# Kernel tuning notes

Measured on AMD Instinct MI355X. Metric: run time of the kernel, lower is better.

Reference implementation:

```python
import jax, jax.numpy as jnp
import numpy as np

RADIUS = 0.2
NSAMPLE = 32


def setup_inputs() -> dict:
    key = jax.random.key(0)
    k1, k2 = jax.random.split(key)
    B, N = 8, 4096
    xyz = jax.random.uniform(k1, (B, N, 3), dtype=jnp.float32)
    xyz_new = jax.random.uniform(k2, (B, N, 3), dtype=jnp.float32)  # ignored by forward, kept for signature fidelity
    return {"xyz": xyz, "xyz_new": xyz_new}


def _ball_query(radius, nsample, xyz, new_xyz):
    # xyz: [B, N, 3] source points; new_xyz: [B, M, 3] query centers.
    # Returns idx: [B, M, nsample] int32, matching pointnet2 CUDA ball_query:
    # first `nsample` indices j (in increasing j order) with ||q - p_j||^2 < r^2;
    # unused slots are filled with the first valid index.
    B, N, _ = xyz.shape
    sq_src = jnp.sum(xyz * xyz, axis=-1)          # [B, N]
    sq_q = jnp.sum(new_xyz * new_xyz, axis=-1)    # [B, M]
    # d2[b, m, n] = ||q_m - p_n||^2
    d2 = sq_q[:, :, None] + sq_src[:, None, :] - 2.0 * jnp.einsum(
        "bmc,bnc->bmn", new_xyz, xyz)             # [B, M, N]
    mask = d2 < (radius * radius)                 # [B, M, N] bool
    # key = index j when within radius, else sentinel N (sorts to the end)
    idx_range = jnp.arange(N, dtype=jnp.int32)
    keys = jnp.where(mask, idx_range[None, None, :], jnp.int32(N))
    sorted_keys = jnp.sort(keys, axis=-1)[..., :nsample]  # [B, M, nsample]
    first = sorted_keys[..., 0:1]                 # first valid index (pad value)
    idx = jnp.where(sorted_keys < N, sorted_keys, first)
    return idx.astype(jnp.int32)


def reference(xyz, xyz_new):
    # Faithful to the module: ball_query(radius, nsample, xyz, xyz) — xyz_new unused.
    return _ball_query(RADIUS, NSAMPLE, xyz, xyz)
```

## Files before the change

kernel.cpp:

```cpp
#include <hip/hip_runtime.h>
#include <cstdint>


#define BQ_N   4096
#define BQ_B   8
#define BQ_NS  32
#define BQ_R2  0.04f

__device__ __forceinline__ float sq_plain(float x, float y, float z) {
    float r, t;
    asm("v_mul_f32 %0, %2, %2\n\t"
        "v_mul_f32 %1, %3, %3\n\t"
        "v_add_f32 %0, %0, %1\n\t"
        "v_mul_f32 %1, %4, %4\n\t"
        "v_add_f32 %0, %0, %1"
        : "=&v"(r), "=&v"(t)
        : "v"(x), "v"(y), "v"(z));
    return r;
}

__device__ __forceinline__ float d2_mixed_s(float qx, float qy, float qz,
                                            float sqq,
                                            float sx, float sy, float sz,
                                            float sqs) {
    float r, t;
    asm("v_mul_f32 %0, %2, %5\n\t"
        "v_fma_f32 %0, %3, %6, %0\n\t"
        "v_fma_f32 %0, %4, %7, %0\n\t"
        "v_add_f32 %0, %0, %0\n\t"
        "v_add_f32 %1, %8, %9\n\t"
        "v_sub_f32 %0, %1, %0"
        : "=&v"(r), "=&v"(t)
        : "s"(qx), "s"(qy), "s"(qz), "v"(sx), "v"(sy), "v"(sz),
          "s"(sqq), "v"(sqs));
    return r;
}

__device__ __forceinline__ float rfl(float v) {
    return __int_as_float(__builtin_amdgcn_readfirstlane(__float_as_int(v)));
}

__device__ __forceinline__ float gfun(float q) {
    float t = fminf(q, 1.0f - q) * 5.0f;
    t = fminf(t, 1.0f);
    return 0.5f + (0.75f - 0.25f * t * t) * t;
}

__device__ __forceinline__ void emit_query(int* orow, int lane, uint64_t word) {
    const int cnt = __popcll(word);
    int incl = cnt;
    #pragma unroll
    for (int off = 1; off < 64; off <<= 1) {
        const int t = __shfl_up(incl, off);
        if (lane >= off) incl += t;
    }
    const int pre   = incl - cnt;
    const int total = __shfl(incl, 63);

    int first;
    const uint64_t nz = __ballot(word != 0ull);
    if (nz == 0ull) {
        first = BQ_N;
    } else {
        const int fl = __builtin_ctzll(nz);
        const uint64_t fw = __shfl(word, fl);
        first = (fl << 6) + __builtin_ctzll(fw);
    }

    uint64_t w = word;
    int pos = pre;
    while (w != 0ull && pos < BQ_NS) {
        const int bit = __builtin_ctzll(w);
        orow[pos] = (lane << 6) + bit;
        w &= (w - 1);
        ++pos;
    }
    if (lane >= total && lane < BQ_NS) orow[lane] = first;
}

__global__ __launch_bounds__(512, 4)
void ball_query_kernel(const float* __restrict__ xyz, int* __restrict__ out)
{
    __shared__ float4 pts[BQ_N];

    const int b     = blockIdx.x >> 6;
    const int qbase = (blockIdx.x & 63) << 6;
    const float* __restrict__ src = xyz + (size_t)b * BQ_N * 3;
    const int lane = threadIdx.x & 63;
    const int wid  = threadIdx.x >> 6;
    int* __restrict__ outb = out + (size_t)(b * BQ_N) * BQ_NS;

    unsigned long long v;
    {
        const int m = qbase + lane;
        const float x = src[3 * m + 0];
        const float y = src[3 * m + 1];
        const float z = src[3 * m + 2];
        const float key = gfun(x) * gfun(y) * gfun(z);
        v = ((unsigned long long)__float_as_uint(key) << 32) | (unsigned)lane;
    }
    #pragma unroll
    for (int k = 2; k <= 64; k <<= 1) {
        #pragma unroll
        for (int j = k >> 1; j > 0; j >>= 1) {
            const unsigned long long o = __shfl_xor(v, j);
            const bool up       = ((lane & k) == 0);
            const bool take_min = (((lane & j) == 0) == up);
            const bool less     = (v < o);
            v = (less == take_min) ? v : o;
        }
    }
    int qlocal[8];
    #pragma unroll
    for (int j = 0; j < 8; ++j)
        qlocal[j] = (int)(__shfl(v, (wid << 3) + j) & 0xffffffffull) & 63;

    for (int j = threadIdx.x; j < BQ_N; j += 512) {
        const float x = src[3 * j + 0];
        const float y = src[3 * j + 1];
        const float z = src[3 * j + 2];
        pts[j] = make_float4(x, y, z, sq_plain(x, y, z));
    }
    __syncthreads();

    float qx[8], qy[8], qz[8], qw[8];
    #pragma unroll
    for (int j = 0; j < 8; ++j) {
        const float4 Qj = pts[qbase + qlocal[j]];
        qx[j] = rfl(Qj.x); qy[j] = rfl(Qj.y);
        qz[j] = rfl(Qj.z); qw[j] = rfl(Qj.w);
    }

    uint64_t W[8] = {0, 0, 0, 0, 0, 0, 0, 0};
    int      F[8] = {0, 0, 0, 0, 0, 0, 0, 0};

    #pragma unroll 1
    for (int c = 0; c < 16; ++c) {
        #pragma unroll
        for (int u = 0; u < 4; ++u) {
            const int k = (c << 2) + u;
            const float4 s = pts[(k << 6) + lane];
            #pragma unroll
            for (int j = 0; j < 8; ++j) {
                const float d2 = d2_mixed_s(qx[j], qy[j], qz[j], qw[j],
                                            s.x, s.y, s.z, s.w);
                const uint64_t bal = __ballot(d2 < BQ_R2);
                if (lane == k) W[j] = bal;
                F[j] += (int)__popcll(bal);
            }
        }
        bool done = true;
        #pragma unroll
        for (int j = 0; j < 8; ++j) done = done && (F[j] >= BQ_NS);
        if (done) break;
    }

    #pragma unroll 1
    for (int j = 0; j < 8; ++j) {
        const int m = qbase + qlocal[j];
        emit_query(outb + (size_t)m * BQ_NS, lane, W[j]);
    }
}

extern "C" void kernel_launch(void* const* d_in, const int* in_sizes, int n_in,
                              void* d_out, int out_size, void* d_ws, size_t ws_size,
                              hipStream_t stream)
{
    const float* xyz = (const float*)d_in[0];
    int* out = (int*)d_out;
    hipLaunchKernelGGL(ball_query_kernel, dim3(BQ_B * 64), dim3(512), 0, stream,
                       xyz, out);
}
```

Measured before the change: 89.59 us.

## Replace per-block bitonic query sort with global per-batch counting sort

A new pre-pass kernel computes, for each query, a key estimating how close it is to the cube boundary. It then counting-sorts every batch's queries into a permutation held in workspace. The main kernel gives each wave 8 queries that are adjacent in this global order, and spreads key ranges across blocks. The aim is that queries sharing a wave have similar neighbour counts, so the early-exit scan stops more uniformly, and that slow boundary queries are balanced across blocks. The cost is an extra launch with only 8 blocks, plus a dependent read of the permutation before the point-loading phase.

```diff
diff --git a/kernel.cpp b/kernel.cpp
--- a/kernel.cpp
+++ b/kernel.cpp
@@ -46,6 +46,52 @@
     return 0.5f + (0.75f - 0.25f * t * t) * t;
 }
 
+__global__ __launch_bounds__(512)
+void bq_sort_kernel(const float* __restrict__ xyz, int* __restrict__ perm)
+{
+    __shared__ int hist[256];
+    __shared__ int scanbuf[256];
+    const int b = blockIdx.x;
+    const float* __restrict__ src = xyz + (size_t)b * BQ_N * 3;
+    int* __restrict__ pb = perm + b * BQ_N;
+    const int t = threadIdx.x;
+
+    if (t < 256) hist[t] = 0;
+    __syncthreads();
+
+    int bins[8];
+    #pragma unroll
+    for (int i = 0; i < 8; ++i) {
+        const int q = t + (i << 9);
+        const float g3 = gfun(src[3 * q + 0]) * gfun(src[3 * q + 1]) *
+                         gfun(src[3 * q + 2]);
+        int bin = (int)(g3 * 255.99f);
+        bin = bin < 0 ? 0 : (bin > 255 ? 255 : bin);
+        bins[i] = bin;
+        atomicAdd(&hist[bin], 1);
+    }
+    __syncthreads();
+
+    if (t < 256) scanbuf[t] = hist[t];
+    __syncthreads();
+    for (int off = 1; off < 256; off <<= 1) {
+        int add = 0;
+        if (t < 256 && t >= off) add = scanbuf[t - off];
+        __syncthreads();
+        if (t < 256) scanbuf[t] += add;
+        __syncthreads();
+    }
+    if (t < 256) hist[t] = scanbuf[t] - hist[t];
+    __syncthreads();
+
+    #pragma unroll
+    for (int i = 0; i < 8; ++i) {
+        const int q = t + (i << 9);
+        const int rank = atomicAdd(&hist[bins[i]], 1);
+        pb[rank] = q;
+    }
+}
+
 __device__ __forceinline__ void emit_query(int* orow, int lane, uint64_t word) {
     const int cnt = __popcll(word);
     int incl = cnt;
@@ -79,41 +125,33 @@
 }
 
 __global__ __launch_bounds__(512, 4)
-void ball_query_kernel(const float* __restrict__ xyz, int* __restrict__ out)
+void ball_query_kernel(const float* __restrict__ xyz,
+                       const int* __restrict__ perm,
+                       int* __restrict__ out)
 {
     __shared__ float4 pts[BQ_N];
 
-    const int b     = blockIdx.x >> 6;
-    const int qbase = (blockIdx.x & 63) << 6;
+    const int b  = blockIdx.x >> 6;
+    const int ib = blockIdx.x & 63;
     const float* __restrict__ src = xyz + (size_t)b * BQ_N * 3;
+    const int* __restrict__ pb = perm + b * BQ_N;
     const int lane = threadIdx.x & 63;
     const int wid  = threadIdx.x >> 6;
     int* __restrict__ outb = out + (size_t)(b * BQ_N) * BQ_NS;
 
-    unsigned long long v;
-    {
-        const int m = qbase + lane;
+    const int G = (wid << 6) + ib;
+    int qidx[8];
+    float qx[8], qy[8], qz[8], qw[8];
+    #pragma unroll
+    for (int j = 0; j < 8; ++j) {
+        const int m = pb[(G << 3) + j];
+        qidx[j] = m;
         const float x = src[3 * m + 0];
         const float y = src[3 * m + 1];
         const float z = src[3 * m + 2];
-        const float key = gfun(x) * gfun(y) * gfun(z);
-        v = ((unsigned long long)__float_as_uint(key) << 32) | (unsigned)lane;
-    }
-    #pragma unroll
-    for (int k = 2; k <= 64; k <<= 1) {
-        #pragma unroll
-        for (int j = k >> 1; j > 0; j >>= 1) {
-            const unsigned long long o = __shfl_xor(v, j);
-            const bool up       = ((lane & k) == 0);
-            const bool take_min = (((lane & j) == 0) == up);
-            const bool less     = (v < o);
-            v = (less == take_min) ? v : o;
-        }
-    }
-    int qlocal[8];
-    #pragma unroll
-    for (int j = 0; j < 8; ++j)
-        qlocal[j] = (int)(__shfl(v, (wid << 3) + j) & 0xffffffffull) & 63;
+        const float w = sq_plain(x, y, z);
+        qx[j] = rfl(x); qy[j] = rfl(y); qz[j] = rfl(z); qw[j] = rfl(w);
+    }
 
     for (int j = threadIdx.x; j < BQ_N; j += 512) {
         const float x = src[3 * j + 0];
@@ -122,14 +160,6 @@
         pts[j] = make_float4(x, y, z, sq_plain(x, y, z));
     }
     __syncthreads();
-
-    float qx[8], qy[8], qz[8], qw[8];
-    #pragma unroll
-    for (int j = 0; j < 8; ++j) {
-        const float4 Qj = pts[qbase + qlocal[j]];
-        qx[j] = rfl(Qj.x); qy[j] = rfl(Qj.y);
-        qz[j] = rfl(Qj.z); qw[j] = rfl(Qj.w);
-    }
 
     uint64_t W[8] = {0, 0, 0, 0, 0, 0, 0, 0};
     int      F[8] = {0, 0, 0, 0, 0, 0, 0, 0};
@@ -156,10 +186,8 @@
     }
 
     #pragma unroll 1
-    for (int j = 0; j < 8; ++j) {
-        const int m = qbase + qlocal[j];
-        emit_query(outb + (size_t)m * BQ_NS, lane, W[j]);
-    }
+    for (int j = 0; j < 8; ++j)
+        emit_query(outb + (size_t)qidx[j] * BQ_NS, lane, W[j]);
 }
 
 extern "C" void kernel_launch(void* const* d_in, const int* in_sizes, int n_in,
@@ -167,7 +195,11 @@
                               hipStream_t stream)
 {
     const float* xyz = (const float*)d_in[0];
-    int* out = (int*)d_out;
+    int* out  = (int*)d_out;
+    int* perm = (int*)d_ws;
+
+    hipLaunchKernelGGL(bq_sort_kernel, dim3(BQ_B), dim3(512), 0, stream,
+                       xyz, perm);
     hipLaunchKernelGGL(ball_query_kernel, dim3(BQ_B * 64), dim3(512), 0, stream,
-                       xyz, out);
-}
+                       xyz, perm, out);
+}
```

Result: slower. 94.14 us (+5.1%).
